# Performance work log

Hardware: AMD Instinct MI355X
Metric: run time of the kernel (lower is better)

The kernel has to match this reference:

```python
import jax, jax.numpy as jnp
import numpy as np

HEAD_SIZE = 64   # baseChn * max_channel_ratio
NUM_HEADS = 2
LEAKY_ALPHA = 0.3  # tf.keras.layers.LeakyReLU default


def setup_inputs() -> dict:
    key = jax.random.key(0)
    ks = jax.random.split(key, 6)
    x = jax.random.normal(ks[0], (96, 48, 512), dtype=jnp.float32)
    y = jax.random.uniform(ks[1], (96, 64, 64), dtype=jnp.float32)
    nItem = jax.random.uniform(ks[2], (96,), dtype=jnp.float32, minval=1.0, maxval=48.0)
    W_proj = jax.random.normal(ks[3], (512, 64), dtype=jnp.float32) * 0.05
    W1 = jax.random.normal(ks[4], (64, 128), dtype=jnp.float32) * 0.1
    W2 = jax.random.normal(ks[5], (2, 1), dtype=jnp.float32)
    return {"x": x, "y": y, "nItem": nItem, "W_proj": W_proj, "W1": W1, "W2": W2}


def reference(x, y, nItem, W_proj, W1, W2):
    # fc_cnn_proj: Dense(64, gelu exact, no bias)
    gallery = jax.nn.gelu(jnp.matmul(x, W_proj), approximate=False)  # [Sx, Nx, 64]
    Sx, Nx, _ = gallery.shape
    Sy, Ny, _ = y.shape
    sqrt_hs = jnp.sqrt(jnp.float32(HEAD_SIZE))
    # shared linear (no bias) then split heads: [S, H, N, hs]
    px = jnp.matmul(gallery, W1).reshape(Sx, Nx, NUM_HEADS, HEAD_SIZE).transpose(0, 2, 1, 3)
    py = jnp.matmul(y, W1).reshape(Sy, Ny, NUM_HEADS, HEAD_SIZE).transpose(0, 2, 1, 3)
    # pairwise cross-set attention maps: [Sy, Sx, H, Ny, Nx]
    att = jnp.einsum('yhmd,xhnd->yxhmn', py, px) / sqrt_hs
    att = jnp.where(att > 0, att, LEAKY_ALPHA * att)
    # reduce over both item axes, normalize by nItem[x] and nItemMax_y
    sc = att.sum(axis=(3, 4)) / nItem[None, :, None] / jnp.float32(Ny)  # [Sy, Sx, H]
    scores = jnp.matmul(sc, W2)  # linear2: Dense(1, no bias) -> [Sy, Sx, 1]
    return scores
```

## Files before the change

kernel.cpp:

```cpp
#include <hip/hip_runtime.h>
#include <hip/hip_bf16.h>


typedef short bf16x8 __attribute__((ext_vector_type(8)));
typedef float f32x4 __attribute__((ext_vector_type(4)));

__device__ __forceinline__ unsigned short f2bf(float v) {
  __hip_bfloat16 b = __float2bfloat16(v);
  return *reinterpret_cast<unsigned short*>(&b);
}

__device__ __forceinline__ bf16x8 load8_cvt(const float* __restrict__ p) {
  f32x4 v0 = *reinterpret_cast<const f32x4*>(p);
  f32x4 v1 = *reinterpret_cast<const f32x4*>(p + 4);
  bf16x8 r;
  r[0] = (short)f2bf(v0[0]); r[1] = (short)f2bf(v0[1]);
  r[2] = (short)f2bf(v0[2]); r[3] = (short)f2bf(v0[3]);
  r[4] = (short)f2bf(v1[0]); r[5] = (short)f2bf(v1[1]);
  r[6] = (short)f2bf(v1[2]); r[7] = (short)f2bf(v1[3]);
  return r;
}

__global__ __launch_bounds__(256) void k_prep(const float* __restrict__ x,
                                              const float* __restrict__ y,
                                              const float* __restrict__ Wp,
                                              const float* __restrict__ W1,
                                              unsigned short* __restrict__ pyf,
                                              unsigned short* __restrict__ pxf) {
  __shared__ unsigned short w1f[8192];
  __shared__ unsigned short wpf[16384];
  __shared__ unsigned short gal[4][1152];
  int t = threadIdx.x;
  int lane = t & 63, w = t >> 6;

#pragma unroll
  for (int it = 0; it < 32; ++it) {
    int idx = it * 256 + t;
    int k = idx >> 7, d = idx & 127;
    int l = (d & 15) + 16 * ((k >> 3) & 3);
    int f = (k >> 5) * 8 + (d >> 4);
    w1f[f * 512 + l * 8 + (k & 7)] = f2bf(W1[idx]);
  }

  if (blockIdx.x >= 72) {
    __syncthreads();
    int yi = blockIdx.x - 72;
    const bf16x8* WF = reinterpret_cast<const bf16x8*>(w1f);
    int row0 = yi * 64 + w * 16 + (lane & 15);
    const float* yb = y + (size_t)row0 * 64 + 8 * (lane >> 4);
    bf16x8 a0 = load8_cvt(yb);
    bf16x8 a1 = load8_cvt(yb + 32);
    f32x4 acc[8];
#pragma unroll
    for (int nt = 0; nt < 8; ++nt) acc[nt] = (f32x4){0.f, 0.f, 0.f, 0.f};
#pragma unroll
    for (int nt = 0; nt < 8; ++nt) {
      acc[nt] = __builtin_amdgcn_mfma_f32_16x16x32_bf16(a0, WF[nt * 64 + lane], acc[nt], 0, 0, 0);
      acc[nt] = __builtin_amdgcn_mfma_f32_16x16x32_bf16(a1, WF[(8 + nt) * 64 + lane], acc[nt], 0, 0, 0);
    }
    int r_hi = (lane >> 4) * 4;
#pragma unroll
    for (int nt = 0; nt < 8; ++nt) {
      int d = nt * 16 + (lane & 15);
      int h = d >> 6, dd = d & 63;
      int kc = dd >> 5, q = (dd >> 3) & 3, i = dd & 7;
#pragma unroll
      for (int j = 0; j < 4; ++j) {
        int m = w * 16 + r_hi + j;
        int mt = m >> 4, rr = m & 15;
        size_t idx = ((size_t)((yi * 2 + h) * 8 + mt * 2 + kc)) * 512 + (rr + (q << 4)) * 8 + i;
        pyf[idx] = f2bf(acc[nt][j]);
      }
    }
  } else {
    int rowbase = blockIdx.x * 64;
#pragma unroll
    for (int it = 0; it < 64; ++it) {
      int idx = it * 256 + t;
      int k = idx >> 6, c = idx & 63;
      int l = (c & 15) + 16 * ((k >> 3) & 3);
      int g = ((k >> 5) & 7) * 4 + (c >> 4);
      wpf[g * 512 + l * 8 + (k & 7)] = f2bf(Wp[idx]);
    }
    __syncthreads();
    const bf16x8* WPF = reinterpret_cast<const bf16x8*>(wpf);
    const bf16x8* WF = reinterpret_cast<const bf16x8*>(w1f);
    int rloc = rowbase + w * 16 + (lane & 15);
    const float* xb = x + (size_t)rloc * 512 + 8 * (lane >> 4);
    f32x4 acc1[4];
#pragma unroll
    for (int nt = 0; nt < 4; ++nt) acc1[nt] = (f32x4){0.f, 0.f, 0.f, 0.f};
#pragma unroll
    for (int kc = 0; kc < 8; ++kc) {
      bf16x8 a = load8_cvt(xb + 32 * kc);
#pragma unroll
      for (int nt = 0; nt < 4; ++nt)
        acc1[nt] = __builtin_amdgcn_mfma_f32_16x16x32_bf16(a, WPF[(kc * 4 + nt) * 64 + lane], acc1[nt], 0, 0, 0);
    }
    __syncthreads();
#pragma unroll
    for (int it = 0; it < 64; ++it) {
      int idx = it * 256 + t;
      int k = idx >> 6, c = idx & 63;
      int l = (c & 15) + 16 * ((k >> 3) & 3);
      int g = ((k >> 5) & 7) * 4 + (c >> 4);
      wpf[g * 512 + l * 8 + (k & 7)] = f2bf(Wp[16384 + idx]);
    }
    __syncthreads();
#pragma unroll
    for (int kc = 0; kc < 8; ++kc) {
      bf16x8 a = load8_cvt(xb + 256 + 32 * kc);
#pragma unroll
      for (int nt = 0; nt < 4; ++nt)
        acc1[nt] = __builtin_amdgcn_mfma_f32_16x16x32_bf16(a, WPF[(kc * 4 + nt) * 64 + lane], acc1[nt], 0, 0, 0);
    }
#pragma unroll
    for (int nt = 0; nt < 4; ++nt)
#pragma unroll
      for (int j = 0; j < 4; ++j) {
        float s = acc1[nt][j];
        float ge = 0.5f * s * (1.0f + erff(s * 0.70710678118654752f));
        int rl = (lane >> 4) * 4 + j;
        int c = nt * 16 + (lane & 15);
        gal[w][rl * 72 + c] = f2bf(ge);
      }
    const unsigned short* gp = &gal[w][(lane & 15) * 72 + 8 * (lane >> 4)];
    bf16x8 g0 = *reinterpret_cast<const bf16x8*>(gp);
    bf16x8 g1 = *reinterpret_cast<const bf16x8*>(gp + 32);
    f32x4 acc2[8];
#pragma unroll
    for (int nt = 0; nt < 8; ++nt) acc2[nt] = (f32x4){0.f, 0.f, 0.f, 0.f};
#pragma unroll
    for (int nt = 0; nt < 8; ++nt) {
      acc2[nt] = __builtin_amdgcn_mfma_f32_16x16x32_bf16(g0, WF[nt * 64 + lane], acc2[nt], 0, 0, 0);
      acc2[nt] = __builtin_amdgcn_mfma_f32_16x16x32_bf16(g1, WF[(8 + nt) * 64 + lane], acc2[nt], 0, 0, 0);
    }
    int r_hi = (lane >> 4) * 4;
#pragma unroll
    for (int nt = 0; nt < 8; ++nt) {
      int d = nt * 16 + (lane & 15);
      int h = d >> 6, dd = d & 63;
      int kc = dd >> 5, q = (dd >> 3) & 3, i = dd & 7;
#pragma unroll
      for (int j = 0; j < 4; ++j) {
        int row = rowbase + w * 16 + r_hi + j;
        int xi = row / 48, n = row % 48;
        int nt3 = n >> 4, rr = n & 15;
        size_t idx = ((size_t)((xi * 2 + h) * 6 + nt3 * 2 + kc)) * 512 + (rr + (q << 4)) * 8 + i;
        pxf[idx] = f2bf(acc2[nt][j]);
      }
    }
  }
}

__global__ __launch_bounds__(256) void k_att(const unsigned short* __restrict__ pyf_u,
                                             const unsigned short* __restrict__ pxf_u,
                                             const float* __restrict__ nItem,
                                             const float* __restrict__ W2,
                                             float* __restrict__ out) {
  int lane = threadIdx.x & 63;
  int w = threadIdx.x >> 6;
  int yi = (blockIdx.x / 24) * 4 + w;
  int xb = (blockIdx.x % 24) * 4;
  const bf16x8* PA = reinterpret_cast<const bf16x8*>(pyf_u);
  const bf16x8* PB = reinterpret_cast<const bf16x8*>(pxf_u);

  f32x4 zero4 = {0.f, 0.f, 0.f, 0.f};
  asm volatile("" : "+v"(zero4));

  bf16x8 a[16];
  size_t abase = (size_t)(yi * 2) * 512 + lane;
#pragma unroll
  for (int f = 0; f < 8; ++f) {
    a[f]     = PA[abase + f * 64];
    a[8 + f] = PA[abase + 512 + f * 64];
  }
  float w2h0 = W2[0], w2h1 = W2[1];
  float res[4];
#pragma unroll
  for (int g = 0; g < 4; ++g) {
    int xi = xb + g;
    f32x4 szw = {0.f, 0.f, 0.f, 0.f};
    f32x4 srw = {0.f, 0.f, 0.f, 0.f};
#pragma unroll
    for (int h = 0; h < 2; ++h) {
      size_t bbase = (size_t)((xi * 2 + h) * 6) * 64 + lane;
      bf16x8 b[6];
#pragma unroll
      for (int f = 0; f < 6; ++f) b[f] = PB[bbase + f * 64];
      float c3 = 0.3f * (h ? w2h1 : w2h0);
      float c7 = 0.7f * (h ? w2h1 : w2h0);
#pragma unroll
      for (int nt = 0; nt < 3; ++nt)
#pragma unroll
        for (int mt = 0; mt < 4; ++mt) {
          f32x4 acc = __builtin_amdgcn_mfma_f32_16x16x32_bf16(a[h * 8 + mt * 2], b[nt * 2], zero4, 0, 0, 0);
          acc = __builtin_amdgcn_mfma_f32_16x16x32_bf16(a[h * 8 + mt * 2 + 1], b[nt * 2 + 1], acc, 0, 0, 0);
          f32x4 mx = {fmaxf(acc[0], 0.f), fmaxf(acc[1], 0.f), fmaxf(acc[2], 0.f), fmaxf(acc[3], 0.f)};
          szw += acc * c3;
          srw += mx * c7;
        }
    }
    f32x4 t4 = szw + srw;
    float tot = (t4[0] + t4[1]) + (t4[2] + t4[3]);
#pragma unroll
    for (int off = 32; off >= 1; off >>= 1) tot += __shfl_xor(tot, off, 64);
    res[g] = tot;
  }
  if (lane == 0) {
#pragma unroll
    for (int g = 0; g < 4; ++g) {
      int xi = xb + g;
      out[yi * 96 + xi] = res[g] / (512.0f * nItem[xi]);
    }
  }
}

extern "C" void kernel_launch(void* const* d_in, const int* in_sizes, int n_in,
                              void* d_out, int out_size, void* d_ws, size_t ws_size,
                              hipStream_t stream) {
  const float* x     = (const float*)d_in[0];
  const float* y     = (const float*)d_in[1];
  const float* nItem = (const float*)d_in[2];
  const float* Wp    = (const float*)d_in[3];
  const float* W1    = (const float*)d_in[4];
  const float* W2    = (const float*)d_in[5];
  float* out = (float*)d_out;

  unsigned short* pyf = (unsigned short*)d_ws;
  unsigned short* pxf = pyf + 786432;

  hipLaunchKernelGGL(k_prep, dim3(168), dim3(256), 0, stream, x, y, Wp, W1, pyf, pxf);
  hipLaunchKernelGGL(k_att, dim3(576), dim3(256), 0, stream, pyf, pxf, nItem, W2, out);
}
```

Before: 34.89 us.

## Fuse prep and attention kernels with a grid-wide flag barrier

Merges the projection and attention kernels into one persistent launch of 384 blocks. The first 168 blocks produce the projections and publish completion flags, and all blocks spin on those flags before running the attention stage. This removes the second kernel launch and the gap between launches. The Wp staging buffer is halved and loaded in four chunks to cut shared memory so two blocks fit per CU, and each attention block now covers 6 x-items instead of 4. The spin barrier only works if all 384 blocks are co-resident, and the last block resets the flags for the next call.

```diff
diff --git a/kernel.cpp b/kernel.cpp
--- a/kernel.cpp
+++ b/kernel.cpp
@@ -4,6 +4,10 @@
 
 typedef short bf16x8 __attribute__((ext_vector_type(8)));
 typedef float f32x4 __attribute__((ext_vector_type(4)));
+
+#define NPROD 168
+#define NBLK  384
+#define MAGIC 0x13572468u
 
 __device__ __forceinline__ unsigned short f2bf(float v) {
   __hip_bfloat16 b = __float2bfloat16(v);
@@ -21,197 +25,205 @@
   return r;
 }
 
-__global__ __launch_bounds__(256) void k_prep(const float* __restrict__ x,
-                                              const float* __restrict__ y,
-                                              const float* __restrict__ Wp,
-                                              const float* __restrict__ W1,
-                                              unsigned short* __restrict__ pyf,
-                                              unsigned short* __restrict__ pxf) {
+__global__ __launch_bounds__(256, 2) void k_fused(const float* __restrict__ x,
+                                                  const float* __restrict__ y,
+                                                  const float* __restrict__ Wp,
+                                                  const float* __restrict__ W1,
+                                                  const float* __restrict__ nItem,
+                                                  const float* __restrict__ W2,
+                                                  unsigned short* __restrict__ pyf,
+                                                  unsigned short* __restrict__ pxf,
+                                                  unsigned int* flags,
+                                                  float* __restrict__ out) {
   __shared__ unsigned short w1f[8192];
-  __shared__ unsigned short wpf[16384];
+  __shared__ unsigned short wpf[8192];
   __shared__ unsigned short gal[4][1152];
   int t = threadIdx.x;
   int lane = t & 63, w = t >> 6;
-
-#pragma unroll
-  for (int it = 0; it < 32; ++it) {
-    int idx = it * 256 + t;
-    int k = idx >> 7, d = idx & 127;
-    int l = (d & 15) + 16 * ((k >> 3) & 3);
-    int f = (k >> 5) * 8 + (d >> 4);
-    w1f[f * 512 + l * 8 + (k & 7)] = f2bf(W1[idx]);
-  }
-
-  if (blockIdx.x >= 72) {
-    __syncthreads();
-    int yi = blockIdx.x - 72;
-    const bf16x8* WF = reinterpret_cast<const bf16x8*>(w1f);
-    int row0 = yi * 64 + w * 16 + (lane & 15);
-    const float* yb = y + (size_t)row0 * 64 + 8 * (lane >> 4);
-    bf16x8 a0 = load8_cvt(yb);
-    bf16x8 a1 = load8_cvt(yb + 32);
-    f32x4 acc[8];
-#pragma unroll
-    for (int nt = 0; nt < 8; ++nt) acc[nt] = (f32x4){0.f, 0.f, 0.f, 0.f};
-#pragma unroll
-    for (int nt = 0; nt < 8; ++nt) {
-      acc[nt] = __builtin_amdgcn_mfma_f32_16x16x32_bf16(a0, WF[nt * 64 + lane], acc[nt], 0, 0, 0);
-      acc[nt] = __builtin_amdgcn_mfma_f32_16x16x32_bf16(a1, WF[(8 + nt) * 64 + lane], acc[nt], 0, 0, 0);
-    }
-    int r_hi = (lane >> 4) * 4;
-#pragma unroll
-    for (int nt = 0; nt < 8; ++nt) {
-      int d = nt * 16 + (lane & 15);
-      int h = d >> 6, dd = d & 63;
-      int kc = dd >> 5, q = (dd >> 3) & 3, i = dd & 7;
-#pragma unroll
-      for (int j = 0; j < 4; ++j) {
-        int m = w * 16 + r_hi + j;
-        int mt = m >> 4, rr = m & 15;
-        size_t idx = ((size_t)((yi * 2 + h) * 8 + mt * 2 + kc)) * 512 + (rr + (q << 4)) * 8 + i;
-        pyf[idx] = f2bf(acc[nt][j]);
-      }
-    }
-  } else {
-    int rowbase = blockIdx.x * 64;
-#pragma unroll
-    for (int it = 0; it < 64; ++it) {
+  int b = blockIdx.x;
+
+  float w2h0 = W2[0], w2h1 = W2[1];
+
+  if (b < NPROD) {
+#pragma unroll
+    for (int it = 0; it < 32; ++it) {
       int idx = it * 256 + t;
-      int k = idx >> 6, c = idx & 63;
-      int l = (c & 15) + 16 * ((k >> 3) & 3);
-      int g = ((k >> 5) & 7) * 4 + (c >> 4);
-      wpf[g * 512 + l * 8 + (k & 7)] = f2bf(Wp[idx]);
-    }
-    __syncthreads();
-    const bf16x8* WPF = reinterpret_cast<const bf16x8*>(wpf);
-    const bf16x8* WF = reinterpret_cast<const bf16x8*>(w1f);
-    int rloc = rowbase + w * 16 + (lane & 15);
-    const float* xb = x + (size_t)rloc * 512 + 8 * (lane >> 4);
-    f32x4 acc1[4];
-#pragma unroll
-    for (int nt = 0; nt < 4; ++nt) acc1[nt] = (f32x4){0.f, 0.f, 0.f, 0.f};
-#pragma unroll
-    for (int kc = 0; kc < 8; ++kc) {
-      bf16x8 a = load8_cvt(xb + 32 * kc);
+      int k = idx >> 7, d = idx & 127;
+      int l = (d & 15) + 16 * ((k >> 3) & 3);
+      int f = (k >> 5) * 8 + (d >> 4);
+      w1f[f * 512 + l * 8 + (k & 7)] = f2bf(W1[idx]);
+    }
+    if (b >= 72) {
+      __syncthreads();
+      int yi = b - 72;
+      const bf16x8* WF = reinterpret_cast<const bf16x8*>(w1f);
+      int row0 = yi * 64 + w * 16 + (lane & 15);
+      const float* yb = y + (size_t)row0 * 64 + 8 * (lane >> 4);
+      bf16x8 a0 = load8_cvt(yb);
+      bf16x8 a1 = load8_cvt(yb + 32);
+      f32x4 acc[8];
+#pragma unroll
+      for (int nt = 0; nt < 8; ++nt) acc[nt] = (f32x4){0.f, 0.f, 0.f, 0.f};
+#pragma unroll
+      for (int nt = 0; nt < 8; ++nt) {
+        acc[nt] = __builtin_amdgcn_mfma_f32_16x16x32_bf16(a0, WF[nt * 64 + lane], acc[nt], 0, 0, 0);
+        acc[nt] = __builtin_amdgcn_mfma_f32_16x16x32_bf16(a1, WF[(8 + nt) * 64 + lane], acc[nt], 0, 0, 0);
+      }
+      int r_hi = (lane >> 4) * 4;
+#pragma unroll
+      for (int nt = 0; nt < 8; ++nt) {
+        int d = nt * 16 + (lane & 15);
+        int h = d >> 6, dd = d & 63;
+        int kc = dd >> 5, q = (dd >> 3) & 3, i = dd & 7;
+#pragma unroll
+        for (int j = 0; j < 4; ++j) {
+          int m = w * 16 + r_hi + j;
+          int mt = m >> 4, rr = m & 15;
+          size_t idx = ((size_t)((yi * 2 + h) * 8 + mt * 2 + kc)) * 512 + (rr + (q << 4)) * 8 + i;
+          pyf[idx] = f2bf(acc[nt][j]);
+        }
+      }
+    } else {
+      int rowbase = b * 64;
+      const bf16x8* WPF = reinterpret_cast<const bf16x8*>(wpf);
+      const bf16x8* WF = reinterpret_cast<const bf16x8*>(w1f);
+      int rloc = rowbase + w * 16 + (lane & 15);
+      const float* xb = x + (size_t)rloc * 512 + 8 * (lane >> 4);
+      f32x4 acc1[4];
+#pragma unroll
+      for (int nt = 0; nt < 4; ++nt) acc1[nt] = (f32x4){0.f, 0.f, 0.f, 0.f};
+#pragma unroll
+      for (int q = 0; q < 4; ++q) {
+        if (q) __syncthreads();
+#pragma unroll
+        for (int it = 0; it < 32; ++it) {
+          int idx = it * 256 + t;
+          int kq = idx >> 6, c = idx & 63;
+          int l = (c & 15) + 16 * ((kq >> 3) & 3);
+          int g = ((kq >> 5) & 3) * 4 + (c >> 4);
+          wpf[g * 512 + l * 8 + (kq & 7)] = f2bf(Wp[(q * 128 + kq) * 64 + c]);
+        }
+        __syncthreads();
+#pragma unroll
+        for (int kk = 0; kk < 4; ++kk) {
+          int kc = q * 4 + kk;
+          bf16x8 a = load8_cvt(xb + 32 * kc);
+#pragma unroll
+          for (int nt = 0; nt < 4; ++nt)
+            acc1[nt] = __builtin_amdgcn_mfma_f32_16x16x32_bf16(a, WPF[(kk * 4 + nt) * 64 + lane], acc1[nt], 0, 0, 0);
+        }
+      }
 #pragma unroll
       for (int nt = 0; nt < 4; ++nt)
-        acc1[nt] = __builtin_amdgcn_mfma_f32_16x16x32_bf16(a, WPF[(kc * 4 + nt) * 64 + lane], acc1[nt], 0, 0, 0);
-    }
-    __syncthreads();
-#pragma unroll
-    for (int it = 0; it < 64; ++it) {
-      int idx = it * 256 + t;
-      int k = idx >> 6, c = idx & 63;
-      int l = (c & 15) + 16 * ((k >> 3) & 3);
-      int g = ((k >> 5) & 7) * 4 + (c >> 4);
-      wpf[g * 512 + l * 8 + (k & 7)] = f2bf(Wp[16384 + idx]);
-    }
-    __syncthreads();
-#pragma unroll
-    for (int kc = 0; kc < 8; ++kc) {
-      bf16x8 a = load8_cvt(xb + 256 + 32 * kc);
-#pragma unroll
-      for (int nt = 0; nt < 4; ++nt)
-        acc1[nt] = __builtin_amdgcn_mfma_f32_16x16x32_bf16(a, WPF[(kc * 4 + nt) * 64 + lane], acc1[nt], 0, 0, 0);
-    }
-#pragma unroll
-    for (int nt = 0; nt < 4; ++nt)
-#pragma unroll
-      for (int j = 0; j < 4; ++j) {
-        float s = acc1[nt][j];
-        float ge = 0.5f * s * (1.0f + erff(s * 0.70710678118654752f));
-        int rl = (lane >> 4) * 4 + j;
-        int c = nt * 16 + (lane & 15);
-        gal[w][rl * 72 + c] = f2bf(ge);
-      }
-    const unsigned short* gp = &gal[w][(lane & 15) * 72 + 8 * (lane >> 4)];
-    bf16x8 g0 = *reinterpret_cast<const bf16x8*>(gp);
-    bf16x8 g1 = *reinterpret_cast<const bf16x8*>(gp + 32);
-    f32x4 acc2[8];
-#pragma unroll
-    for (int nt = 0; nt < 8; ++nt) acc2[nt] = (f32x4){0.f, 0.f, 0.f, 0.f};
-#pragma unroll
-    for (int nt = 0; nt < 8; ++nt) {
-      acc2[nt] = __builtin_amdgcn_mfma_f32_16x16x32_bf16(g0, WF[nt * 64 + lane], acc2[nt], 0, 0, 0);
-      acc2[nt] = __builtin_amdgcn_mfma_f32_16x16x32_bf16(g1, WF[(8 + nt) * 64 + lane], acc2[nt], 0, 0, 0);
-    }
-    int r_hi = (lane >> 4) * 4;
-#pragma unroll
-    for (int nt = 0; nt < 8; ++nt) {
-      int d = nt * 16 + (lane & 15);
-      int h = d >> 6, dd = d & 63;
-      int kc = dd >> 5, q = (dd >> 3) & 3, i = dd & 7;
-#pragma unroll
-      for (int j = 0; j < 4; ++j) {
-        int row = rowbase + w * 16 + r_hi + j;
-        int xi = row / 48, n = row % 48;
-        int nt3 = n >> 4, rr = n & 15;
-        size_t idx = ((size_t)((xi * 2 + h) * 6 + nt3 * 2 + kc)) * 512 + (rr + (q << 4)) * 8 + i;
-        pxf[idx] = f2bf(acc2[nt][j]);
-      }
-    }
-  }
-}
-
-__global__ __launch_bounds__(256) void k_att(const unsigned short* __restrict__ pyf_u,
-                                             const unsigned short* __restrict__ pxf_u,
-                                             const float* __restrict__ nItem,
-                                             const float* __restrict__ W2,
-                                             float* __restrict__ out) {
-  int lane = threadIdx.x & 63;
-  int w = threadIdx.x >> 6;
-  int yi = (blockIdx.x / 24) * 4 + w;
-  int xb = (blockIdx.x % 24) * 4;
-  const bf16x8* PA = reinterpret_cast<const bf16x8*>(pyf_u);
-  const bf16x8* PB = reinterpret_cast<const bf16x8*>(pxf_u);
-
-  f32x4 zero4 = {0.f, 0.f, 0.f, 0.f};
-  asm volatile("" : "+v"(zero4));
-
-  bf16x8 a[16];
-  size_t abase = (size_t)(yi * 2) * 512 + lane;
-#pragma unroll
-  for (int f = 0; f < 8; ++f) {
-    a[f]     = PA[abase + f * 64];
-    a[8 + f] = PA[abase + 512 + f * 64];
-  }
-  float w2h0 = W2[0], w2h1 = W2[1];
-  float res[4];
-#pragma unroll
-  for (int g = 0; g < 4; ++g) {
-    int xi = xb + g;
-    f32x4 szw = {0.f, 0.f, 0.f, 0.f};
-    f32x4 srw = {0.f, 0.f, 0.f, 0.f};
-#pragma unroll
-    for (int h = 0; h < 2; ++h) {
-      size_t bbase = (size_t)((xi * 2 + h) * 6) * 64 + lane;
-      bf16x8 b[6];
-#pragma unroll
-      for (int f = 0; f < 6; ++f) b[f] = PB[bbase + f * 64];
-      float c3 = 0.3f * (h ? w2h1 : w2h0);
-      float c7 = 0.7f * (h ? w2h1 : w2h0);
-#pragma unroll
-      for (int nt = 0; nt < 3; ++nt)
-#pragma unroll
-        for (int mt = 0; mt < 4; ++mt) {
-          f32x4 acc = __builtin_amdgcn_mfma_f32_16x16x32_bf16(a[h * 8 + mt * 2], b[nt * 2], zero4, 0, 0, 0);
-          acc = __builtin_amdgcn_mfma_f32_16x16x32_bf16(a[h * 8 + mt * 2 + 1], b[nt * 2 + 1], acc, 0, 0, 0);
-          f32x4 mx = {fmaxf(acc[0], 0.f), fmaxf(acc[1], 0.f), fmaxf(acc[2], 0.f), fmaxf(acc[3], 0.f)};
-          szw += acc * c3;
-          srw += mx * c7;
-        }
-    }
-    f32x4 t4 = szw + srw;
-    float tot = (t4[0] + t4[1]) + (t4[2] + t4[3]);
-#pragma unroll
-    for (int off = 32; off >= 1; off >>= 1) tot += __shfl_xor(tot, off, 64);
-    res[g] = tot;
-  }
-  if (lane == 0) {
-#pragma unroll
-    for (int g = 0; g < 4; ++g) {
-      int xi = xb + g;
-      out[yi * 96 + xi] = res[g] / (512.0f * nItem[xi]);
+#pragma unroll
+        for (int j = 0; j < 4; ++j) {
+          float s = acc1[nt][j];
+          float ge = 0.5f * s * (1.0f + erff(s * 0.70710678118654752f));
+          int rl = (lane >> 4) * 4 + j;
+          int c = nt * 16 + (lane & 15);
+          gal[w][rl * 72 + c] = f2bf(ge);
+        }
+      const unsigned short* gp = &gal[w][(lane & 15) * 72 + 8 * (lane >> 4)];
+      bf16x8 g0 = *reinterpret_cast<const bf16x8*>(gp);
+      bf16x8 g1 = *reinterpret_cast<const bf16x8*>(gp + 32);
+      f32x4 acc2[8];
+#pragma unroll
+      for (int nt = 0; nt < 8; ++nt) acc2[nt] = (f32x4){0.f, 0.f, 0.f, 0.f};
+#pragma unroll
+      for (int nt = 0; nt < 8; ++nt) {
+        acc2[nt] = __builtin_amdgcn_mfma_f32_16x16x32_bf16(g0, WF[nt * 64 + lane], acc2[nt], 0, 0, 0);
+        acc2[nt] = __builtin_amdgcn_mfma_f32_16x16x32_bf16(g1, WF[(8 + nt) * 64 + lane], acc2[nt], 0, 0, 0);
+      }
+      int r_hi = (lane >> 4) * 4;
+#pragma unroll
+      for (int nt = 0; nt < 8; ++nt) {
+        int d = nt * 16 + (lane & 15);
+        int h = d >> 6, dd = d & 63;
+        int kc = dd >> 5, q2 = (dd >> 3) & 3, i = dd & 7;
+#pragma unroll
+        for (int j = 0; j < 4; ++j) {
+          int row = rowbase + w * 16 + r_hi + j;
+          int xi = row / 48, n = row % 48;
+          int nt3 = n >> 4, rr = n & 15;
+          size_t idx = ((size_t)((xi * 2 + h) * 6 + nt3 * 2 + kc)) * 512 + (rr + (q2 << 4)) * 8 + i;
+          pxf[idx] = f2bf(acc2[nt][j]);
+        }
+      }
+    }
+  }
+
+  __syncthreads();
+  if (b < NPROD && t == 0)
+    __hip_atomic_store(&flags[b], MAGIC, __ATOMIC_RELEASE, __HIP_MEMORY_SCOPE_AGENT);
+  for (;;) {
+    unsigned v = (t < NPROD)
+        ? __hip_atomic_load(&flags[t], __ATOMIC_RELAXED, __HIP_MEMORY_SCOPE_AGENT)
+        : MAGIC;
+    if (__syncthreads_count((int)(v == MAGIC)) == 256) break;
+  }
+  __threadfence();
+
+  {
+    int yb2 = b >> 4, xq = b & 15;
+    int yi = yb2 * 4 + w;
+    int xi0 = xq * 6;
+    const bf16x8* PA = reinterpret_cast<const bf16x8*>(pyf);
+    const bf16x8* PB = reinterpret_cast<const bf16x8*>(pxf);
+
+    f32x4 zero4 = {0.f, 0.f, 0.f, 0.f};
+    asm volatile("" : "+v"(zero4));
+
+    bf16x8 a[16];
+    size_t abase = (size_t)(yi * 2) * 512 + lane;
+#pragma unroll
+    for (int f = 0; f < 8; ++f) {
+      a[f]     = PA[abase + f * 64];
+      a[8 + f] = PA[abase + 512 + f * 64];
+    }
+    float res[6];
+#pragma unroll
+    for (int g = 0; g < 6; ++g) {
+      int xi = xi0 + g;
+      f32x4 szw = {0.f, 0.f, 0.f, 0.f};
+      f32x4 srw = {0.f, 0.f, 0.f, 0.f};
+#pragma unroll
+      for (int h = 0; h < 2; ++h) {
+        size_t bbase = (size_t)((xi * 2 + h) * 6) * 64 + lane;
+        bf16x8 bb[6];
+#pragma unroll
+        for (int f = 0; f < 6; ++f) bb[f] = PB[bbase + f * 64];
+        float c3 = 0.3f * (h ? w2h1 : w2h0);
+        float c7 = 0.7f * (h ? w2h1 : w2h0);
+#pragma unroll
+        for (int nt = 0; nt < 3; ++nt)
+#pragma unroll
+          for (int mt = 0; mt < 4; ++mt) {
+            f32x4 acc = __builtin_amdgcn_mfma_f32_16x16x32_bf16(a[h * 8 + mt * 2], bb[nt * 2], zero4, 0, 0, 0);
+            acc = __builtin_amdgcn_mfma_f32_16x16x32_bf16(a[h * 8 + mt * 2 + 1], bb[nt * 2 + 1], acc, 0, 0, 0);
+            f32x4 mx = {fmaxf(acc[0], 0.f), fmaxf(acc[1], 0.f), fmaxf(acc[2], 0.f), fmaxf(acc[3], 0.f)};
+            szw += acc * c3;
+            srw += mx * c7;
+          }
+      }
+      f32x4 t4 = szw + srw;
+      float tot = (t4[0] + t4[1]) + (t4[2] + t4[3]);
+#pragma unroll
+      for (int off = 32; off >= 1; off >>= 1) tot += __shfl_xor(tot, off, 64);
+      res[g] = tot;
+    }
+    if (lane == 0) {
+#pragma unroll
+      for (int g = 0; g < 6; ++g)
+        out[yi * 96 + xi0 + g] = res[g] / (512.0f * nItem[xi0 + g]);
+    }
+  }
+
+  __syncthreads();
+  if (t == 0) {
+    unsigned n = __hip_atomic_fetch_add(&flags[NPROD], 1u, __ATOMIC_ACQ_REL, __HIP_MEMORY_SCOPE_AGENT);
+    if (n == NBLK - 1) {
+      for (int i = 0; i <= NPROD; ++i)
+        __hip_atomic_store(&flags[i], 0u, __ATOMIC_RELAXED, __HIP_MEMORY_SCOPE_AGENT);
     }
   }
 }
@@ -229,7 +241,8 @@
 
   unsigned short* pyf = (unsigned short*)d_ws;
   unsigned short* pxf = pyf + 786432;
-
-  hipLaunchKernelGGL(k_prep, dim3(168), dim3(256), 0, stream, x, y, Wp, W1, pyf, pxf);
-  hipLaunchKernelGGL(k_att, dim3(576), dim3(256), 0, stream, pyf, pxf, nItem, W2, out);
-}
+  unsigned int* flags = (unsigned int*)(pxf + 589824);
+
+  hipLaunchKernelGGL(k_fused, dim3(NBLK), dim3(256), 0, stream,
+                     x, y, Wp, W1, nItem, W2, pyf, pxf, flags, out);
+}
```

New measurement: 72.41 us. 108% more time.
